# Optimization experiments

Hardware: AMD Instinct MI355X
Metric: run time of the kernel (lower is better)

The kernel has to match this reference:

```python
import jax, jax.numpy as jnp
import numpy as np

B, L, CIN, COUT, NCH = 64, 8192, 128, 128, 64


def setup_inputs() -> dict:
    key = jax.random.key(0)
    k1, k2, k3, k4 = jax.random.split(key, 4)
    x = jax.random.normal(k1, (B, L, CIN), dtype=jnp.float32)
    channels = jax.random.randint(k2, (L,), 0, NCH, dtype=jnp.int64)
    # kaiming_uniform-ish scale for weight, uniform bias in [-1/sqrt(fan_in), 1/sqrt(fan_in)]
    wbound = jnp.sqrt(1.0 / CIN)
    weight = jax.random.uniform(k3, (NCH, COUT, CIN), dtype=jnp.float32, minval=-wbound, maxval=wbound)
    bias = jax.random.uniform(k4, (NCH, COUT), dtype=jnp.float32, minval=-wbound, maxval=wbound)
    return {"x": x, "channels": channels, "weight": weight, "bias": bias}


def reference(x, channels, weight, bias):
    # Gather per-site weights: (L, Cout, Cin), then batched matmul over L.
    Wg = weight[channels]            # (L, Cout, Cin)
    bg = bias[channels]              # (L, Cout)
    y = jnp.einsum('blc,loc->blo', x, Wg)  # (B, L, Cout)
    y = y + bg                        # broadcast over B
    y = jnp.tanh(y)                   # activation=True
    y = y + x                         # residual mode 1 (Cout == Cin)
    return (y, channels)
```

## Files before the change

### kernel.cpp

```cpp
#include <hip/hip_runtime.h>
#include <hip/hip_bf16.h>


#define BB   64
#define LL   8192
#define CIN  128
#define COUT 128
#define NCH  64

#define PA 136

typedef __bf16 bf16x4 __attribute__((ext_vector_type(4)));
typedef __bf16 bf16x8 __attribute__((ext_vector_type(8)));
typedef float  f32x4  __attribute__((ext_vector_type(4)));

__device__ __forceinline__ int load_channel(const int* __restrict__ ch32, int l) {
    bool is64 = true;
    #pragma unroll
    for (int i = 1; i < 32; i += 2) is64 = is64 && (ch32[i] == 0);
    return is64 ? ch32[2 * l] : ch32[l];
}

__global__ void convert_w_kernel(const float* __restrict__ w,
                                 __hip_bfloat16* __restrict__ wb)
{
    int i = (blockIdx.x * 256 + threadIdx.x) * 8;
    float4 a = *(const float4*)(w + i);
    float4 b = *(const float4*)(w + i + 4);
    bf16x8 r = { (__bf16)a.x, (__bf16)a.y, (__bf16)a.z, (__bf16)a.w,
                 (__bf16)b.x, (__bf16)b.y, (__bf16)b.z, (__bf16)b.w };
    *(bf16x8*)(wb + i) = r;
}

template<bool PRE>
__global__ __launch_bounds__(256, 5) void gather_gemm_kernel(
    const float* __restrict__ x,
    const int* __restrict__ channels,
    const float* __restrict__ weight,
    const __hip_bfloat16* __restrict__ wbf,
    const float* __restrict__ bias,
    float* __restrict__ out)
{
    __shared__ __align__(16) __hip_bfloat16 sA[BB * PA];

    const int l = blockIdx.x;
    const int t = threadIdx.x;
    const int ch = load_channel(channels, l);

    const float* xl = x + (size_t)l * CIN;
    #pragma unroll
    for (int i = 0; i < 8; ++i) {
        int c   = t + 256 * i;
        int row = c >> 5;
        int cc  = c & 31;
        float4 v = *(const float4*)(xl + (size_t)row * ((size_t)LL * CIN) + cc * 4);
        bf16x4 b4 = { (__bf16)v.x, (__bf16)v.y, (__bf16)v.z, (__bf16)v.w };
        *(bf16x4*)(&sA[row * PA + cc * 4]) = b4;
    }

    const int wave = t >> 6;
    const int lane = t & 63;
    const int n0   = lane & 15;
    const int quad = lane >> 4;

    bf16x8 wfr[2][4];
    if constexpr (PRE) {
        const __hip_bfloat16* wbc = wbf + (size_t)ch * (COUT * CIN);
        #pragma unroll
        for (int oi = 0; oi < 2; ++oi) {
            int n = wave * 32 + oi * 16 + n0;
            #pragma unroll
            for (int ks = 0; ks < 4; ++ks)
                wfr[oi][ks] = *(const bf16x8*)(wbc + n * CIN + ks * 32 + quad * 8);
        }
    }
    __syncthreads();

    if constexpr (!PRE) {
        const float* wc = weight + (size_t)ch * (COUT * CIN);
        #pragma unroll
        for (int oi = 0; oi < 2; ++oi) {
            int n = wave * 32 + oi * 16 + n0;
            #pragma unroll
            for (int ks = 0; ks < 4; ++ks) {
                const float* p = wc + n * CIN + ks * 32 + quad * 8;
                float4 a = *(const float4*)(p);
                float4 b = *(const float4*)(p + 4);
                wfr[oi][ks] = (bf16x8){ (__bf16)a.x, (__bf16)a.y, (__bf16)a.z, (__bf16)a.w,
                                        (__bf16)b.x, (__bf16)b.y, (__bf16)b.z, (__bf16)b.w };
            }
        }
    }

    f32x4 acc[2][4];
    #pragma unroll
    for (int oi = 0; oi < 2; ++oi)
        #pragma unroll
        for (int bj = 0; bj < 4; ++bj)
            acc[oi][bj] = (f32x4){0.f, 0.f, 0.f, 0.f};

    #pragma unroll
    for (int ks = 0; ks < 4; ++ks) {
        const int k = ks * 32 + quad * 8;
        bf16x8 afr[4];
        #pragma unroll
        for (int bj = 0; bj < 4; ++bj)
            afr[bj] = *(const bf16x8*)(&sA[(bj * 16 + n0) * PA + k]);
        #pragma unroll
        for (int oi = 0; oi < 2; ++oi)
            #pragma unroll
            for (int bj = 0; bj < 4; ++bj)
                acc[oi][bj] = __builtin_amdgcn_mfma_f32_16x16x32_bf16(
                    wfr[oi][ks], afr[bj], acc[oi][bj], 0, 0, 0);
    }

    #pragma unroll
    for (int oi = 0; oi < 2; ++oi) {
        const int o0 = wave * 32 + oi * 16 + quad * 4;
        const f32x4 bv = *(const f32x4*)(bias + ch * COUT + o0);
        #pragma unroll
        for (int bj = 0; bj < 4; ++bj) {
            const int b = bj * 16 + n0;
            const bf16x4 rb = *(const bf16x4*)(&sA[b * PA + o0]);
            f32x4 v;
            #pragma unroll
            for (int r = 0; r < 4; ++r) {
                float vv = acc[oi][bj][r] + bv[r];
                float e  = __expf(2.0f * vv);
                float th = 1.0f - 2.0f * __builtin_amdgcn_rcpf(e + 1.0f);
                v[r] = th + (float)rb[r];
            }
            *(f32x4*)(&out[((size_t)b * LL + l) * COUT + o0]) = v;
        }
    }
}

__global__ void chan_out_kernel(const int* __restrict__ channels,
                                float* __restrict__ out)
{
    int i = blockIdx.x * blockDim.x + threadIdx.x;
    int v = load_channel(channels, i);
    if (i < LL)
        out[(size_t)BB * LL * COUT + i] = (float)v;
}

extern "C" void kernel_launch(void* const* d_in, const int* in_sizes, int n_in,
                              void* d_out, int out_size, void* d_ws, size_t ws_size,
                              hipStream_t stream) {
    const float* x        = (const float*)d_in[0];
    const int*   channels = (const int*)d_in[1];
    const float* weight   = (const float*)d_in[2];
    const float* bias     = (const float*)d_in[3];
    float*       out      = (float*)d_out;

    const size_t wbytes = (size_t)NCH * COUT * CIN * sizeof(__hip_bfloat16);
    if (ws_size >= wbytes) {
        __hip_bfloat16* wbf = (__hip_bfloat16*)d_ws;
        convert_w_kernel<<<dim3(512), dim3(256), 0, stream>>>(weight, wbf);
        gather_gemm_kernel<true><<<dim3(LL), dim3(256), 0, stream>>>(
            x, channels, weight, wbf, bias, out);
    } else {
        gather_gemm_kernel<false><<<dim3(LL), dim3(256), 0, stream>>>(
            x, channels, weight, nullptr, bias, out);
    }
    chan_out_kernel<<<dim3(LL / 256), dim3(256), 0, stream>>>(channels, out);
}
```

Baseline: 491.1 us.

## Process four sequence positions per block with double-buffered x staging

Each block now handles four consecutive L positions instead of one, cutting the grid by four. While the current position's MFMA and epilogue run, it prefetches the next position's x slice into registers, then writes it to a second LDS buffer. The intent is to hide global load latency and amortise block launch and channel-detection overhead. In exchange it doubles LDS use, raises register pressure, and drops the occupancy hint from 5 to 4 blocks, which can reduce the latency hiding that came from many resident blocks.

```diff
diff --git a/kernel.cpp b/kernel.cpp
--- a/kernel.cpp
+++ b/kernel.cpp
@@ -7,19 +7,18 @@
 #define CIN  128
 #define COUT 128
 #define NCH  64
-
-#define PA 136
+#define LB   4
+#define PA   136
 
 typedef __bf16 bf16x4 __attribute__((ext_vector_type(4)));
 typedef __bf16 bf16x8 __attribute__((ext_vector_type(8)));
 typedef float  f32x4  __attribute__((ext_vector_type(4)));
 
-__device__ __forceinline__ int load_channel(const int* __restrict__ ch32, int l) {
-    bool is64 = true;
-    #pragma unroll
-    for (int i = 1; i < 32; i += 2) is64 = is64 && (ch32[i] == 0);
-    return is64 ? ch32[2 * l] : ch32[l];
-}
+#define LGKM_BARRIER()                                          \
+    do {                                                        \
+        asm volatile("s_waitcnt lgkmcnt(0)" ::: "memory");      \
+        __builtin_amdgcn_s_barrier();                           \
+    } while (0)
 
 __global__ void convert_w_kernel(const float* __restrict__ w,
                                  __hip_bfloat16* __restrict__ wb)
@@ -33,7 +32,7 @@
 }
 
 template<bool PRE>
-__global__ __launch_bounds__(256, 5) void gather_gemm_kernel(
+__global__ __launch_bounds__(256, 4) void gather_gemm_kernel(
     const float* __restrict__ x,
     const int* __restrict__ channels,
     const float* __restrict__ weight,
@@ -41,22 +40,18 @@
     const float* __restrict__ bias,
     float* __restrict__ out)
 {
-    __shared__ __align__(16) __hip_bfloat16 sA[BB * PA];
-
-    const int l = blockIdx.x;
-    const int t = threadIdx.x;
-    const int ch = load_channel(channels, l);
-
-    const float* xl = x + (size_t)l * CIN;
-    #pragma unroll
-    for (int i = 0; i < 8; ++i) {
-        int c   = t + 256 * i;
-        int row = c >> 5;
-        int cc  = c & 31;
-        float4 v = *(const float4*)(xl + (size_t)row * ((size_t)LL * CIN) + cc * 4);
-        bf16x4 b4 = { (__bf16)v.x, (__bf16)v.y, (__bf16)v.z, (__bf16)v.w };
-        *(bf16x4*)(&sA[row * PA + cc * 4]) = b4;
-    }
+    __shared__ __align__(16) __hip_bfloat16 sA[2][BB * PA];
+
+    const int l0 = blockIdx.x * LB;
+    const int t  = threadIdx.x;
+
+    bool is64 = true;
+    #pragma unroll
+    for (int i = 1; i < 32; i += 2) is64 = is64 && (channels[i] == 0);
+    int chs[LB];
+    #pragma unroll
+    for (int j = 0; j < LB; ++j)
+        chs[j] = is64 ? channels[2 * (l0 + j)] : channels[l0 + j];
 
     const int wave = t >> 6;
     const int lane = t & 63;
@@ -64,82 +59,128 @@
     const int quad = lane >> 4;
 
     bf16x8 wfr[2][4];
-    if constexpr (PRE) {
-        const __hip_bfloat16* wbc = wbf + (size_t)ch * (COUT * CIN);
+    float4  xr[8];
+
+#define LOAD_W(ch_)                                                           \
+    if constexpr (PRE) {                                                      \
+        const __hip_bfloat16* wbc = wbf + (size_t)(ch_) * (COUT * CIN);       \
+        _Pragma("unroll")                                                     \
+        for (int oi = 0; oi < 2; ++oi) {                                      \
+            int n = wave * 32 + oi * 16 + n0;                                 \
+            _Pragma("unroll")                                                 \
+            for (int ks = 0; ks < 4; ++ks)                                    \
+                wfr[oi][ks] = *(const bf16x8*)(wbc + n * CIN + ks * 32 + quad * 8); \
+        }                                                                     \
+    } else {                                                                  \
+        const float* wc = weight + (size_t)(ch_) * (COUT * CIN);              \
+        _Pragma("unroll")                                                     \
+        for (int oi = 0; oi < 2; ++oi) {                                      \
+            int n = wave * 32 + oi * 16 + n0;                                 \
+            _Pragma("unroll")                                                 \
+            for (int ks = 0; ks < 4; ++ks) {                                  \
+                const float* p = wc + n * CIN + ks * 32 + quad * 8;           \
+                float4 a = *(const float4*)(p);                               \
+                float4 b = *(const float4*)(p + 4);                           \
+                wfr[oi][ks] = (bf16x8){(__bf16)a.x, (__bf16)a.y, (__bf16)a.z, (__bf16)a.w, \
+                                       (__bf16)b.x, (__bf16)b.y, (__bf16)b.z, (__bf16)b.w}; \
+            }                                                                 \
+        }                                                                     \
+    }
+
+#define LOAD_X(lidx)                                                          \
+    {                                                                         \
+        const float* xl = x + (size_t)(lidx) * CIN;                           \
+        _Pragma("unroll")                                                     \
+        for (int i = 0; i < 8; ++i) {                                         \
+            int c = t + 256 * i, row = c >> 5, cc = c & 31;                   \
+            xr[i] = *(const float4*)(xl + (size_t)row * ((size_t)LL * CIN) + cc * 4); \
+        }                                                                     \
+    }
+
+#define STAGE_X(buf)                                                          \
+    {                                                                         \
+        _Pragma("unroll")                                                     \
+        for (int i = 0; i < 8; ++i) {                                         \
+            int c = t + 256 * i, row = c >> 5, cc = c & 31;                   \
+            bf16x4 b4 = {(__bf16)xr[i].x, (__bf16)xr[i].y,                    \
+                         (__bf16)xr[i].z, (__bf16)xr[i].w};                   \
+            *(bf16x4*)(&sA[buf][row * PA + cc * 4]) = b4;                     \
+        }                                                                     \
+    }
+
+    LOAD_W(chs[0]);
+    LOAD_X(l0);
+    STAGE_X(0);
+    LGKM_BARRIER();
+
+    #pragma unroll
+    for (int j = 0; j < LB; ++j) {
+        const int cur = j & 1;
+        if (j > 0) { LOAD_W(chs[j]); }
+        if (j + 1 < LB) { LOAD_X(l0 + j + 1); }
+
+        f32x4 acc[2][4];
+        #pragma unroll
+        for (int oi = 0; oi < 2; ++oi)
+            #pragma unroll
+            for (int bj = 0; bj < 4; ++bj)
+                acc[oi][bj] = (f32x4){0.f, 0.f, 0.f, 0.f};
+
+        #pragma unroll
+        for (int ks = 0; ks < 4; ++ks) {
+            const int k = ks * 32 + quad * 8;
+            bf16x8 afr[4];
+            #pragma unroll
+            for (int bj = 0; bj < 4; ++bj)
+                afr[bj] = *(const bf16x8*)(&sA[cur][(bj * 16 + n0) * PA + k]);
+            #pragma unroll
+            for (int oi = 0; oi < 2; ++oi)
+                #pragma unroll
+                for (int bj = 0; bj < 4; ++bj)
+                    acc[oi][bj] = __builtin_amdgcn_mfma_f32_16x16x32_bf16(
+                        wfr[oi][ks], afr[bj], acc[oi][bj], 0, 0, 0);
+        }
+
+        const int l  = l0 + j;
+        const int ch = chs[j];
         #pragma unroll
         for (int oi = 0; oi < 2; ++oi) {
-            int n = wave * 32 + oi * 16 + n0;
-            #pragma unroll
-            for (int ks = 0; ks < 4; ++ks)
-                wfr[oi][ks] = *(const bf16x8*)(wbc + n * CIN + ks * 32 + quad * 8);
-        }
-    }
-    __syncthreads();
-
-    if constexpr (!PRE) {
-        const float* wc = weight + (size_t)ch * (COUT * CIN);
-        #pragma unroll
-        for (int oi = 0; oi < 2; ++oi) {
-            int n = wave * 32 + oi * 16 + n0;
-            #pragma unroll
-            for (int ks = 0; ks < 4; ++ks) {
-                const float* p = wc + n * CIN + ks * 32 + quad * 8;
-                float4 a = *(const float4*)(p);
-                float4 b = *(const float4*)(p + 4);
-                wfr[oi][ks] = (bf16x8){ (__bf16)a.x, (__bf16)a.y, (__bf16)a.z, (__bf16)a.w,
-                                        (__bf16)b.x, (__bf16)b.y, (__bf16)b.z, (__bf16)b.w };
+            const int o0 = wave * 32 + oi * 16 + quad * 4;
+            const f32x4 bv = *(const f32x4*)(bias + ch * COUT + o0);
+            #pragma unroll
+            for (int bj = 0; bj < 4; ++bj) {
+                const int b = bj * 16 + n0;
+                const bf16x4 rb = *(const bf16x4*)(&sA[cur][b * PA + o0]);
+                f32x4 v;
+                #pragma unroll
+                for (int r = 0; r < 4; ++r) {
+                    float vv = acc[oi][bj][r] + bv[r];
+                    float e  = __expf(2.0f * vv);
+                    float th = 1.0f - 2.0f * __builtin_amdgcn_rcpf(e + 1.0f);
+                    v[r] = th + (float)rb[r];
+                }
+                *(f32x4*)(&out[((size_t)b * LL + l) * COUT + o0]) = v;
             }
         }
-    }
-
-    f32x4 acc[2][4];
-    #pragma unroll
-    for (int oi = 0; oi < 2; ++oi)
-        #pragma unroll
-        for (int bj = 0; bj < 4; ++bj)
-            acc[oi][bj] = (f32x4){0.f, 0.f, 0.f, 0.f};
-
-    #pragma unroll
-    for (int ks = 0; ks < 4; ++ks) {
-        const int k = ks * 32 + quad * 8;
-        bf16x8 afr[4];
-        #pragma unroll
-        for (int bj = 0; bj < 4; ++bj)
-            afr[bj] = *(const bf16x8*)(&sA[(bj * 16 + n0) * PA + k]);
-        #pragma unroll
-        for (int oi = 0; oi < 2; ++oi)
-            #pragma unroll
-            for (int bj = 0; bj < 4; ++bj)
-                acc[oi][bj] = __builtin_amdgcn_mfma_f32_16x16x32_bf16(
-                    wfr[oi][ks], afr[bj], acc[oi][bj], 0, 0, 0);
-    }
-
-    #pragma unroll
-    for (int oi = 0; oi < 2; ++oi) {
-        const int o0 = wave * 32 + oi * 16 + quad * 4;
-        const f32x4 bv = *(const f32x4*)(bias + ch * COUT + o0);
-        #pragma unroll
-        for (int bj = 0; bj < 4; ++bj) {
-            const int b = bj * 16 + n0;
-            const bf16x4 rb = *(const bf16x4*)(&sA[b * PA + o0]);
-            f32x4 v;
-            #pragma unroll
-            for (int r = 0; r < 4; ++r) {
-                float vv = acc[oi][bj][r] + bv[r];
-                float e  = __expf(2.0f * vv);
-                float th = 1.0f - 2.0f * __builtin_amdgcn_rcpf(e + 1.0f);
-                v[r] = th + (float)rb[r];
-            }
-            *(f32x4*)(&out[((size_t)b * LL + l) * COUT + o0]) = v;
+
+        if (j + 1 < LB) {
+            STAGE_X(cur ^ 1);
+            LGKM_BARRIER();
         }
     }
+#undef LOAD_W
+#undef LOAD_X
+#undef STAGE_X
 }
 
 __global__ void chan_out_kernel(const int* __restrict__ channels,
                                 float* __restrict__ out)
 {
+    bool is64 = true;
+    #pragma unroll
+    for (int i = 1; i < 32; i += 2) is64 = is64 && (channels[i] == 0);
     int i = blockIdx.x * blockDim.x + threadIdx.x;
-    int v = load_channel(channels, i);
+    int v = is64 ? channels[2 * i] : channels[i];
     if (i < LL)
         out[(size_t)BB * LL * COUT + i] = (float)v;
 }
@@ -157,10 +198,10 @@
     if (ws_size >= wbytes) {
         __hip_bfloat16* wbf = (__hip_bfloat16*)d_ws;
         convert_w_kernel<<<dim3(512), dim3(256), 0, stream>>>(weight, wbf);
-        gather_gemm_kernel<true><<<dim3(LL), dim3(256), 0, stream>>>(
+        gather_gemm_kernel<true><<<dim3(LL / LB), dim3(256), 0, stream>>>(
             x, channels, weight, wbf, bias, out);
     } else {
-        gather_gemm_kernel<false><<<dim3(LL), dim3(256), 0, stream>>>(
+        gather_gemm_kernel<false><<<dim3(LL / LB), dim3(256), 0, stream>>>(
             x, channels, weight, nullptr, bias, out);
     }
     chan_out_kernel<<<dim3(LL / 256), dim3(256), 0, stream>>>(channels, out);
```

Result: slower. 513.4 us (+4.5%).

## Process 16 sites per block with double-buffered async global-to-LDS x staging

Applied to the files above, without the earlier changes.

Each block now handles 16 consecutive L positions instead of one, with x tiles copied straight into LDS as fp32 through global_load_lds into two buffers. The load for the next site overlaps the MFMA work and epilogue of the current one. An XOR swizzle on the LDS layout is meant to avoid bank conflicts. This removes per-block launch and sync overhead and the register round-trip for x, but doubles LDS use (64KB fp32 per block), lowers occupancy to 2 blocks per CU, and shrinks the grid to 512 blocks.

```diff
diff --git a/kernel.cpp b/kernel.cpp
--- a/kernel.cpp
+++ b/kernel.cpp
@@ -7,19 +7,14 @@
 #define CIN  128
 #define COUT 128
 #define NCH  64
-
-#define PA 136
-
-typedef __bf16 bf16x4 __attribute__((ext_vector_type(4)));
+#define LB   16
+#define GRID (LL / LB)
+
 typedef __bf16 bf16x8 __attribute__((ext_vector_type(8)));
 typedef float  f32x4  __attribute__((ext_vector_type(4)));
 
-__device__ __forceinline__ int load_channel(const int* __restrict__ ch32, int l) {
-    bool is64 = true;
-    #pragma unroll
-    for (int i = 1; i < 32; i += 2) is64 = is64 && (ch32[i] == 0);
-    return is64 ? ch32[2 * l] : ch32[l];
-}
+typedef const __attribute__((address_space(1))) void gvoid_t;
+typedef __attribute__((address_space(3))) void svoid_t;
 
 __global__ void convert_w_kernel(const float* __restrict__ w,
                                  __hip_bfloat16* __restrict__ wb)
@@ -33,7 +28,7 @@
 }
 
 template<bool PRE>
-__global__ __launch_bounds__(256, 5) void gather_gemm_kernel(
+__global__ __launch_bounds__(256, 2) void gather_gemm_kernel(
     const float* __restrict__ x,
     const int* __restrict__ channels,
     const float* __restrict__ weight,
@@ -41,105 +36,147 @@
     const float* __restrict__ bias,
     float* __restrict__ out)
 {
-    __shared__ __align__(16) __hip_bfloat16 sA[BB * PA];
-
-    const int l = blockIdx.x;
-    const int t = threadIdx.x;
-    const int ch = load_channel(channels, l);
-
-    const float* xl = x + (size_t)l * CIN;
+    __shared__ __align__(16) float sX[2][BB * CIN];
+
+    const int l0   = blockIdx.x * LB;
+    const int t    = threadIdx.x;
+    const int wv   = t >> 6;
+    const int ln   = t & 63;
+    const int n0   = ln & 15;
+    const int quad = ln >> 4;
+
+    bool is64 = true;
     #pragma unroll
-    for (int i = 0; i < 8; ++i) {
-        int c   = t + 256 * i;
-        int row = c >> 5;
-        int cc  = c & 31;
-        float4 v = *(const float4*)(xl + (size_t)row * ((size_t)LL * CIN) + cc * 4);
-        bf16x4 b4 = { (__bf16)v.x, (__bf16)v.y, (__bf16)v.z, (__bf16)v.w };
-        *(bf16x4*)(&sA[row * PA + cc * 4]) = b4;
-    }
-
-    const int wave = t >> 6;
-    const int lane = t & 63;
-    const int n0   = lane & 15;
-    const int quad = lane >> 4;
-
-    bf16x8 wfr[2][4];
-    if constexpr (PRE) {
-        const __hip_bfloat16* wbc = wbf + (size_t)ch * (COUT * CIN);
+    for (int i = 1; i < 32; i += 2) is64 = is64 && (channels[i] == 0);
+
+#define STAGE(buf, lidx)                                                      \
+    do {                                                                      \
+        const float* xl_ = x + (size_t)(lidx) * CIN;                          \
+        _Pragma("unroll")                                                     \
+        for (int i_ = 0; i_ < 8; ++i_) {                                      \
+            int D0 = i_ * 256 + wv * 64;       \
+            int d  = D0 + ln;                                                 \
+            int r  = d >> 5;                                 \
+            int g  = d & 31;                                 \
+            int gs = g ^ (r & 7);                                             \
+            const float* src_ = xl_ + (size_t)r * ((size_t)LL * CIN) + gs * 4;\
+            __builtin_amdgcn_global_load_lds((gvoid_t*)src_,                  \
+                (svoid_t*)&sX[buf][D0 * 4], 16, 0, 0);                        \
+        }                                                                     \
+    } while (0)
+
+    int ch_cur = is64 ? channels[2 * l0] : channels[l0];
+    STAGE(0, l0);
+    asm volatile("s_waitcnt vmcnt(0)" ::: "memory");
+    __builtin_amdgcn_s_barrier();
+
+    #pragma unroll 2
+    for (int j = 0; j < LB; ++j) {
+        const int cur = j & 1;
+        const float* sXc = sX[cur];
+        const int lnext = l0 + j + 1;
+        int ch_nxt = 0;
+        if (j + 1 < LB)
+            ch_nxt = is64 ? channels[2 * lnext] : channels[lnext];
+
+        bf16x8 wfr[2][4];
+        f32x4  bv[2];
+        if constexpr (PRE) {
+            const __hip_bfloat16* wbc = wbf + (size_t)ch_cur * (COUT * CIN);
+            #pragma unroll
+            for (int oi = 0; oi < 2; ++oi) {
+                const int n = wv * 32 + oi * 16 + n0;
+                #pragma unroll
+                for (int ks = 0; ks < 4; ++ks)
+                    wfr[oi][ks] = *(const bf16x8*)(wbc + n * CIN + ks * 32 + quad * 8);
+                bv[oi] = *(const f32x4*)(bias + ch_cur * COUT + wv * 32 + oi * 16 + quad * 4);
+            }
+        } else {
+            const float* wc = weight + (size_t)ch_cur * (COUT * CIN);
+            #pragma unroll
+            for (int oi = 0; oi < 2; ++oi) {
+                const int n = wv * 32 + oi * 16 + n0;
+                #pragma unroll
+                for (int ks = 0; ks < 4; ++ks) {
+                    const float* p = wc + n * CIN + ks * 32 + quad * 8;
+                    float4 a = *(const float4*)(p);
+                    float4 b = *(const float4*)(p + 4);
+                    wfr[oi][ks] = (bf16x8){(__bf16)a.x, (__bf16)a.y, (__bf16)a.z, (__bf16)a.w,
+                                           (__bf16)b.x, (__bf16)b.y, (__bf16)b.z, (__bf16)b.w};
+                }
+                bv[oi] = *(const f32x4*)(bias + ch_cur * COUT + wv * 32 + oi * 16 + quad * 4);
+            }
+        }
+        __builtin_amdgcn_sched_barrier(0);
+        if (j + 1 < LB) STAGE(cur ^ 1, lnext);
+        __builtin_amdgcn_sched_barrier(0);
+
+        f32x4 acc[2][4];
+        #pragma unroll
+        for (int oi = 0; oi < 2; ++oi)
+            #pragma unroll
+            for (int bj = 0; bj < 4; ++bj)
+                acc[oi][bj] = (f32x4){0.f, 0.f, 0.f, 0.f};
+
+        #pragma unroll
+        for (int ks = 0; ks < 4; ++ks) {
+            bf16x8 afr[4];
+            #pragma unroll
+            for (int bj = 0; bj < 4; ++bj) {
+                const int m  = bj * 16 + n0;
+                const int s  = m & 7;
+                const int g0 = ks * 8 + quad * 2;
+                f32x4 a0 = *(const f32x4*)&sXc[m * CIN + ((g0    ) ^ s) * 4];
+                f32x4 a1 = *(const f32x4*)&sXc[m * CIN + ((g0 + 1) ^ s) * 4];
+                afr[bj] = (bf16x8){(__bf16)a0.x, (__bf16)a0.y, (__bf16)a0.z, (__bf16)a0.w,
+                                   (__bf16)a1.x, (__bf16)a1.y, (__bf16)a1.z, (__bf16)a1.w};
+            }
+            #pragma unroll
+            for (int oi = 0; oi < 2; ++oi)
+                #pragma unroll
+                for (int bj = 0; bj < 4; ++bj)
+                    acc[oi][bj] = __builtin_amdgcn_mfma_f32_16x16x32_bf16(
+                        wfr[oi][ks], afr[bj], acc[oi][bj], 0, 0, 0);
+        }
+
+        const int l = l0 + j;
         #pragma unroll
         for (int oi = 0; oi < 2; ++oi) {
-            int n = wave * 32 + oi * 16 + n0;
-            #pragma unroll
-            for (int ks = 0; ks < 4; ++ks)
-                wfr[oi][ks] = *(const bf16x8*)(wbc + n * CIN + ks * 32 + quad * 8);
-        }
+            const int o0 = wv * 32 + oi * 16 + quad * 4;
+            const int gr = o0 >> 2;
+            #pragma unroll
+            for (int bj = 0; bj < 4; ++bj) {
+                const int b = bj * 16 + n0;
+                f32x4 res = *(const f32x4*)&sXc[b * CIN + (gr ^ (b & 7)) * 4];
+                f32x4 v;
+                #pragma unroll
+                for (int r = 0; r < 4; ++r) {
+                    float vv = acc[oi][bj][r] + bv[oi][r];
+                    float e  = __expf(2.0f * vv);
+                    float th = 1.0f - 2.0f * __builtin_amdgcn_rcpf(e + 1.0f);
+                    v[r] = th + res[r];
+                }
+                *(f32x4*)(&out[((size_t)b * LL + l) * COUT + o0]) = v;
+            }
+        }
+
+        if (j + 1 < LB) {
+            asm volatile("s_waitcnt vmcnt(8)" ::: "memory");
+            __builtin_amdgcn_s_barrier();
+        }
+        ch_cur = ch_nxt;
     }
-    __syncthreads();
-
-    if constexpr (!PRE) {
-        const float* wc = weight + (size_t)ch * (COUT * CIN);
-        #pragma unroll
-        for (int oi = 0; oi < 2; ++oi) {
-            int n = wave * 32 + oi * 16 + n0;
-            #pragma unroll
-            for (int ks = 0; ks < 4; ++ks) {
-                const float* p = wc + n * CIN + ks * 32 + quad * 8;
-                float4 a = *(const float4*)(p);
-                float4 b = *(const float4*)(p + 4);
-                wfr[oi][ks] = (bf16x8){ (__bf16)a.x, (__bf16)a.y, (__bf16)a.z, (__bf16)a.w,
-                                        (__bf16)b.x, (__bf16)b.y, (__bf16)b.z, (__bf16)b.w };
-            }
-        }
-    }
-
-    f32x4 acc[2][4];
-    #pragma unroll
-    for (int oi = 0; oi < 2; ++oi)
-        #pragma unroll
-        for (int bj = 0; bj < 4; ++bj)
-            acc[oi][bj] = (f32x4){0.f, 0.f, 0.f, 0.f};
-
-    #pragma unroll
-    for (int ks = 0; ks < 4; ++ks) {
-        const int k = ks * 32 + quad * 8;
-        bf16x8 afr[4];
-        #pragma unroll
-        for (int bj = 0; bj < 4; ++bj)
-            afr[bj] = *(const bf16x8*)(&sA[(bj * 16 + n0) * PA + k]);
-        #pragma unroll
-        for (int oi = 0; oi < 2; ++oi)
-            #pragma unroll
-            for (int bj = 0; bj < 4; ++bj)
-                acc[oi][bj] = __builtin_amdgcn_mfma_f32_16x16x32_bf16(
-                    wfr[oi][ks], afr[bj], acc[oi][bj], 0, 0, 0);
-    }
-
-    #pragma unroll
-    for (int oi = 0; oi < 2; ++oi) {
-        const int o0 = wave * 32 + oi * 16 + quad * 4;
-        const f32x4 bv = *(const f32x4*)(bias + ch * COUT + o0);
-        #pragma unroll
-        for (int bj = 0; bj < 4; ++bj) {
-            const int b = bj * 16 + n0;
-            const bf16x4 rb = *(const bf16x4*)(&sA[b * PA + o0]);
-            f32x4 v;
-            #pragma unroll
-            for (int r = 0; r < 4; ++r) {
-                float vv = acc[oi][bj][r] + bv[r];
-                float e  = __expf(2.0f * vv);
-                float th = 1.0f - 2.0f * __builtin_amdgcn_rcpf(e + 1.0f);
-                v[r] = th + (float)rb[r];
-            }
-            *(f32x4*)(&out[((size_t)b * LL + l) * COUT + o0]) = v;
-        }
-    }
+#undef STAGE
 }
 
 __global__ void chan_out_kernel(const int* __restrict__ channels,
                                 float* __restrict__ out)
 {
+    bool is64 = true;
+    #pragma unroll
+    for (int i = 1; i < 32; i += 2) is64 = is64 && (channels[i] == 0);
     int i = blockIdx.x * blockDim.x + threadIdx.x;
-    int v = load_channel(channels, i);
+    int v = is64 ? channels[2 * i] : channels[i];
     if (i < LL)
         out[(size_t)BB * LL * COUT + i] = (float)v;
 }
@@ -157,10 +194,10 @@
     if (ws_size >= wbytes) {
         __hip_bfloat16* wbf = (__hip_bfloat16*)d_ws;
         convert_w_kernel<<<dim3(512), dim3(256), 0, stream>>>(weight, wbf);
-        gather_gemm_kernel<true><<<dim3(LL), dim3(256), 0, stream>>>(
+        gather_gemm_kernel<true><<<dim3(GRID), dim3(256), 0, stream>>>(
             x, channels, weight, wbf, bias, out);
     } else {
-        gather_gemm_kernel<false><<<dim3(LL), dim3(256), 0, stream>>>(
+        gather_gemm_kernel<false><<<dim3(GRID), dim3(256), 0, stream>>>(
             x, channels, weight, nullptr, bias, out);
     }
     chan_out_kernel<<<dim3(LL / 256), dim3(256), 0, stream>>>(channels, out);
```

Measured after the change: 508.9 us. +3.6%, slower.
